# Performance work log

Hardware: AMD Instinct MI355X
Metric: run time of the kernel (lower is better)

## Reference

```python
import jax, jax.numpy as jnp
import numpy as np

N_NODES = 10000
N_EDGES = 640000
IN_FEATS = 128
H_FEATS1 = 128
NUM_OUTPUTS = 64


def setup_inputs() -> dict:
    key = jax.random.key(0)
    k0, k1, k2, k3, k4 = jax.random.split(key, 5)
    in_feat = jax.random.normal(k0, (N_NODES, IN_FEATS), dtype=jnp.float32)
    src = jax.random.randint(k1, (N_EDGES,), 0, N_NODES, dtype=jnp.int64)
    dst = jax.random.randint(k2, (N_EDGES,), 0, N_NODES, dtype=jnp.int64)
    W1 = jax.random.normal(k3, (IN_FEATS, H_FEATS1), dtype=jnp.float32) * 0.05
    b1 = jnp.zeros((H_FEATS1,), dtype=jnp.float32)
    W2 = jax.random.normal(k4, (H_FEATS1, NUM_OUTPUTS), dtype=jnp.float32) * 0.05
    b2 = jnp.zeros((NUM_OUTPUTS,), dtype=jnp.float32)
    return {"in_feat": in_feat, "src": src, "dst": dst,
            "W1": W1, "b1": b1, "W2": W2, "b2": b2}


def _graph_conv(src, dst, x, W, b):
    # DGL GraphConv with norm='both': out = D_out^{-1/2} A^T-agg D_in^{-1/2} x W + b
    n = x.shape[0]
    ones = jnp.ones((src.shape[0],), dtype=x.dtype)
    deg_out = jnp.clip(jax.ops.segment_sum(ones, src, num_segments=n), 1.0)
    deg_in = jnp.clip(jax.ops.segment_sum(ones, dst, num_segments=n), 1.0)
    h = x * jax.lax.rsqrt(deg_out)[:, None]            # src-side normalization
    agg = jax.ops.segment_sum(h[src], dst, num_segments=n)  # SpMM: sum over in-edges
    agg = agg * jax.lax.rsqrt(deg_in)[:, None]         # dst-side normalization
    return agg @ W + b


def reference(in_feat, src, dst, W1, b1, W2, b2):
    h = _graph_conv(src, dst, in_feat, W1, b1)
    h = jax.nn.relu(h)  # dropout=0 -> identity
    return _graph_conv(src, dst, h, W2, b2)
```

## Files before the change

kernel.cpp:

```cpp
#include <hip/hip_runtime.h>

#define NFEAT 128
#define NOUT  64
#define PCAP  128
#define HB    256

__global__ void hist_kernel(const int* __restrict__ src, const int* __restrict__ dst,
                            unsigned char* __restrict__ hist_src,
                            unsigned char* __restrict__ hist_dst,
                            unsigned int* __restrict__ pe, int nN, int nE) {
    extern __shared__ int bins[];
    int b = blockIdx.x;
    int per = (nE + HB - 1) / HB;
    int lo = b * per, hi = min(lo + per, nE);
    for (int i = threadIdx.x; i < nN; i += blockDim.x) bins[i] = 0;
    __syncthreads();
    for (int e = lo + threadIdx.x; e < hi; e += blockDim.x) {
        int s = src[e], d = dst[e];
        atomicAdd(&bins[d], 1);
        atomicAdd(&bins[s], 0x10000);
        pe[e] = (unsigned int)(unsigned short)s | ((unsigned int)d << 16);
    }
    __syncthreads();
    for (int i = threadIdx.x; i < nN; i += blockDim.x) {
        int v = bins[i];
        hist_dst[(size_t)b * nN + i] = (unsigned char)min(v & 0xFFFF, 255);
        hist_src[(size_t)b * nN + i] = (unsigned char)min(v >> 16, 255);
    }
}

__global__ void offsets_kernel(const unsigned char* __restrict__ hist_src,
                               const unsigned char* __restrict__ hist_dst,
                               unsigned char* __restrict__ base_rel,
                               unsigned short* __restrict__ deg_in,
                               float* __restrict__ rs_in, float* __restrict__ rs_out, int nN) {
    int tid = blockIdx.x * blockDim.x + threadIdx.x;
    if (tid < nN) {
        int i = tid;
        int run = 0;
#pragma unroll 16
        for (int b = 0; b < HB; b++) {
            base_rel[(size_t)b * nN + i] = (unsigned char)min(run, 255);
            run += hist_dst[(size_t)b * nN + i];
        }
        deg_in[i] = (unsigned short)min(run, PCAP);
        rs_in[i] = rsqrtf(fmaxf((float)run, 1.0f));
    } else if (tid < 2 * nN) {
        int i = tid - nN;
        int to = 0;
#pragma unroll 16
        for (int b = 0; b < HB; b++) to += hist_src[(size_t)b * nN + i];
        rs_out[i] = rsqrtf(fmaxf((float)to, 1.0f));
    }
}

__global__ void scatter_kernel(const unsigned int* __restrict__ pe,
                               const unsigned char* __restrict__ base_rel,
                               unsigned short* __restrict__ csr, int nN, int nE) {
    extern __shared__ int cur[];
    int b = blockIdx.x;
    int per = (nE + HB - 1) / HB;
    int lo = b * per, hi = min(lo + per, nE);
    for (int i = threadIdx.x; i < nN; i += blockDim.x)
        cur[i] = base_rel[(size_t)b * nN + i];
    __syncthreads();
    for (int e = lo + threadIdx.x; e < hi; e += blockDim.x) {
        unsigned int v = pe[e];
        int s = v & 0xFFFF, d = v >> 16;
        int pos = atomicAdd(&cur[d], 1);
        if (pos < PCAP)
            csr[(size_t)d * PCAP + pos] = (unsigned short)s;
    }
}

__global__ void gather1_kernel(const unsigned short* __restrict__ deg_in,
                               const unsigned short* __restrict__ csr,
                               const float* __restrict__ x, const float* __restrict__ rs_out,
                               const float* __restrict__ rs_in,
                               float* __restrict__ t, int nN) {
    __shared__ unsigned short eids[4][PCAP];
    __shared__ float rsv[4][PCAP];
    int tid = threadIdx.x;
    int w = tid >> 6, lane = tid & 63;
    int i = blockIdx.x * 4 + w;
    int n = deg_in[i];
    ((unsigned int*)eids[w])[lane] = ((const unsigned int*)(csr + (size_t)i * PCAP))[lane];
    __syncthreads();
    for (int e = lane; e < n; e += 64) rsv[w][e] = rs_out[eids[w][e]];
    __syncthreads();

    const float4* xv = (const float4*)x;
    int quad = lane >> 4;
    int g = lane & 15;
    float s_in = rs_in[i];
#pragma unroll
    for (int p = 0; p < 2; p++) {
        int gg = g + 16 * p;
        float4 acc = {0.f, 0.f, 0.f, 0.f};
        int e = quad;
        for (; e + 12 < n; e += 16) {
            int s0 = eids[w][e],     s1 = eids[w][e + 4];
            int s2 = eids[w][e + 8], s3 = eids[w][e + 12];
            float f0 = rsv[w][e],     f1 = rsv[w][e + 4];
            float f2 = rsv[w][e + 8], f3 = rsv[w][e + 12];
            float4 v0 = xv[(size_t)s0 * 32 + gg];
            float4 v1 = xv[(size_t)s1 * 32 + gg];
            float4 v2 = xv[(size_t)s2 * 32 + gg];
            float4 v3 = xv[(size_t)s3 * 32 + gg];
            acc.x += v0.x * f0 + v1.x * f1 + v2.x * f2 + v3.x * f3;
            acc.y += v0.y * f0 + v1.y * f1 + v2.y * f2 + v3.y * f3;
            acc.z += v0.z * f0 + v1.z * f1 + v2.z * f2 + v3.z * f3;
            acc.w += v0.w * f0 + v1.w * f1 + v2.w * f2 + v3.w * f3;
        }
        for (; e + 4 < n; e += 8) {
            int s0 = eids[w][e], s1 = eids[w][e + 4];
            float f0 = rsv[w][e], f1 = rsv[w][e + 4];
            float4 v0 = xv[(size_t)s0 * 32 + gg];
            float4 v1 = xv[(size_t)s1 * 32 + gg];
            acc.x += v0.x * f0 + v1.x * f1;
            acc.y += v0.y * f0 + v1.y * f1;
            acc.z += v0.z * f0 + v1.z * f1;
            acc.w += v0.w * f0 + v1.w * f1;
        }
        for (; e < n; e += 4) {
            int s0 = eids[w][e];
            float f0 = rsv[w][e];
            float4 v0 = xv[(size_t)s0 * 32 + gg];
            acc.x += v0.x * f0; acc.y += v0.y * f0; acc.z += v0.z * f0; acc.w += v0.w * f0;
        }
#pragma unroll
        for (int d = 16; d <= 32; d <<= 1) {
            acc.x += __shfl_xor(acc.x, d);
            acc.y += __shfl_xor(acc.y, d);
            acc.z += __shfl_xor(acc.z, d);
            acc.w += __shfl_xor(acc.w, d);
        }
        if (lane < 16) {
            acc.x *= s_in; acc.y *= s_in; acc.z *= s_in; acc.w *= s_in;
            ((float4*)(t + (size_t)i * NFEAT))[gg] = acc;
        }
    }
}

#define NPB 16
__global__ void mlp_kernel(const float* __restrict__ t_in, const float* __restrict__ rs_out,
                           const float* __restrict__ W1, const float* __restrict__ b1,
                           const float* __restrict__ W2, float* __restrict__ z, int nN) {
    __shared__ float ts[NPB][NFEAT];
    __shared__ float h1[NPB][NFEAT];
    int i0 = blockIdx.x * NPB;
    int tid = threadIdx.x;
    for (int t2 = tid; t2 < NPB * NFEAT; t2 += 256)
        ts[t2 >> 7][t2 & 127] = t_in[(size_t)i0 * NFEAT + t2];
    __syncthreads();
    {
        int j = tid & 127;
        int g = (tid >> 7) * 8;
        float a[8];
        float b = b1[j];
#pragma unroll
        for (int u = 0; u < 8; u++) a[u] = b;
#pragma unroll 8
        for (int k = 0; k < NFEAT; k++) {
            float w = W1[k * NFEAT + j];
#pragma unroll
            for (int u = 0; u < 8; u++) a[u] += ts[g + u][k] * w;
        }
#pragma unroll
        for (int u = 0; u < 8; u++) h1[g + u][j] = fmaxf(a[u], 0.0f);
    }
    __syncthreads();
    {
        int j2 = tid & 63;
        int g2 = (tid >> 6) * 4;
        float c[4] = {0.f, 0.f, 0.f, 0.f};
#pragma unroll 8
        for (int k = 0; k < NFEAT; k++) {
            float w = W2[k * NOUT + j2];
#pragma unroll
            for (int u = 0; u < 4; u++) c[u] += h1[g2 + u][k] * w;
        }
#pragma unroll
        for (int u = 0; u < 4; u++)
            z[(size_t)(i0 + g2 + u) * NOUT + j2] = c[u] * rs_out[i0 + g2 + u];
    }
}

__global__ void gather2_kernel(const unsigned short* __restrict__ deg_in,
                               const unsigned short* __restrict__ csr,
                               const float* __restrict__ z, const float* __restrict__ rs_in,
                               const float* __restrict__ b2, float* __restrict__ out, int nN) {
    __shared__ unsigned short eids[4][PCAP];
    int tid = threadIdx.x;
    int w = tid >> 6, lane = tid & 63;
    int i = blockIdx.x * 4 + w;
    int n = deg_in[i];
    ((unsigned int*)eids[w])[lane] = ((const unsigned int*)(csr + (size_t)i * PCAP))[lane];
    __syncthreads();

    const float4* zv = (const float4*)z;
    int quad = lane >> 4;
    int g = lane & 15;
    float4 acc = {0.f, 0.f, 0.f, 0.f};
    int e = quad;
    for (; e + 12 < n; e += 16) {
        int s0 = eids[w][e],     s1 = eids[w][e + 4];
        int s2 = eids[w][e + 8], s3 = eids[w][e + 12];
        float4 v0 = zv[(size_t)s0 * 16 + g];
        float4 v1 = zv[(size_t)s1 * 16 + g];
        float4 v2 = zv[(size_t)s2 * 16 + g];
        float4 v3 = zv[(size_t)s3 * 16 + g];
        acc.x += v0.x + v1.x + v2.x + v3.x;
        acc.y += v0.y + v1.y + v2.y + v3.y;
        acc.z += v0.z + v1.z + v2.z + v3.z;
        acc.w += v0.w + v1.w + v2.w + v3.w;
    }
    for (; e + 4 < n; e += 8) {
        float4 v0 = zv[(size_t)eids[w][e] * 16 + g];
        float4 v1 = zv[(size_t)eids[w][e + 4] * 16 + g];
        acc.x += v0.x + v1.x; acc.y += v0.y + v1.y;
        acc.z += v0.z + v1.z; acc.w += v0.w + v1.w;
    }
    for (; e < n; e += 4) {
        float4 v0 = zv[(size_t)eids[w][e] * 16 + g];
        acc.x += v0.x; acc.y += v0.y; acc.z += v0.z; acc.w += v0.w;
    }
#pragma unroll
    for (int d = 16; d <= 32; d <<= 1) {
        acc.x += __shfl_xor(acc.x, d);
        acc.y += __shfl_xor(acc.y, d);
        acc.z += __shfl_xor(acc.z, d);
        acc.w += __shfl_xor(acc.w, d);
    }
    if (lane < 16) {
        float s = rs_in[i];
        float4 bb = ((const float4*)b2)[g];
        acc.x = acc.x * s + bb.x; acc.y = acc.y * s + bb.y;
        acc.z = acc.z * s + bb.z; acc.w = acc.w * s + bb.w;
        ((float4*)(out + (size_t)i * NOUT))[g] = acc;
    }
}

extern "C" void kernel_launch(void* const* d_in, const int* in_sizes, int n_in,
                              void* d_out, int out_size, void* d_ws, size_t ws_size,
                              hipStream_t stream) {
    const float* x  = (const float*)d_in[0];
    const int* src  = (const int*)d_in[1];
    const int* dst  = (const int*)d_in[2];
    const float* W1 = (const float*)d_in[3];
    const float* b1 = (const float*)d_in[4];
    const float* W2 = (const float*)d_in[5];
    const float* b2 = (const float*)d_in[6];
    float* out = (float*)d_out;

    const int nN = in_sizes[0] / NFEAT;
    const int nE = in_sizes[1];

    char* p = (char*)d_ws;
    unsigned char* hist_src = (unsigned char*)p; p += (size_t)HB * nN;
    unsigned char* hist_dst = (unsigned char*)p; p += (size_t)HB * nN;
    unsigned char* base_rel = (unsigned char*)p; p += (size_t)HB * nN;
    unsigned int*  pe       = (unsigned int*)p;  p += (size_t)nE * 4;
    unsigned short* csr     = (unsigned short*)p; p += (size_t)nN * PCAP * 2;
    unsigned short* deg_in  = (unsigned short*)p; p += (size_t)nN * 2;
    float* rs_in  = (float*)p; p += (size_t)nN * sizeof(float);
    float* rs_out = (float*)p; p += (size_t)nN * sizeof(float);
    float* t = (float*)p; p += (size_t)nN * NFEAT * sizeof(float);
    float* z = (float*)p; p += (size_t)nN * NOUT * sizeof(float);

    hist_kernel<<<HB, 256, (size_t)nN * sizeof(int), stream>>>(
        src, dst, hist_src, hist_dst, pe, nN, nE);
    offsets_kernel<<<(2 * nN + 255) / 256, 256, 0, stream>>>(
        hist_src, hist_dst, base_rel, deg_in, rs_in, rs_out, nN);
    scatter_kernel<<<HB, 256, (size_t)nN * sizeof(int), stream>>>(
        pe, base_rel, csr, nN, nE);
    gather1_kernel<<<nN / 4, 256, 0, stream>>>(deg_in, csr, x, rs_out, rs_in, t, nN);
    mlp_kernel<<<nN / NPB, 256, 0, stream>>>(t, rs_out, W1, b1, W2, z, nN);
    gather2_kernel<<<nN / 4, 256, 0, stream>>>(deg_in, csr, z, rs_in, b2, out, nN);
}
```

Measured before the change: 160.8 us.

## Store gathered node features in bf16 to halve SpMM gather traffic

The input features are converted to packed bf16 inside the histogram kernel, and the second-layer projected features are written as bf16 by the MLP kernel. Both gather kernels now read 16-byte packed bf16 rows, unpack them to fp32 and accumulate in fp32, with the lane mapping reworked to match. This targets the random-access gather bandwidth that dominates the SpMM stages. In exchange it adds a conversion pass and bf16 rounding error on the aggregated features.

Measured after the change: 161.0 us. Within noise of the previous version (+0.1%).

```diff
diff --git a/kernel.cpp b/kernel.cpp
--- a/kernel.cpp
+++ b/kernel.cpp
@@ -5,10 +5,22 @@
 #define PCAP  128
 #define HB    256
 
+__device__ __forceinline__ unsigned int f2bf(float f) {
+    union { float f; unsigned int u; } v; v.f = f;
+    return (v.u + 0x7FFFu + ((v.u >> 16) & 1u)) >> 16;
+}
+__device__ __forceinline__ void unpack2(unsigned int u, float& lo, float& hi) {
+    union { unsigned int u; float f; } a, b;
+    a.u = u << 16; b.u = u & 0xFFFF0000u;
+    lo = a.f; hi = b.f;
+}
+
 __global__ void hist_kernel(const int* __restrict__ src, const int* __restrict__ dst,
+                            const float* __restrict__ x,
                             unsigned char* __restrict__ hist_src,
                             unsigned char* __restrict__ hist_dst,
-                            unsigned int* __restrict__ pe, int nN, int nE) {
+                            unsigned int* __restrict__ pe,
+                            unsigned int* __restrict__ xh, int nN, int nE) {
     extern __shared__ int bins[];
     int b = blockIdx.x;
     int per = (nE + HB - 1) / HB;
@@ -26,6 +38,11 @@
         int v = bins[i];
         hist_dst[(size_t)b * nN + i] = (unsigned char)min(v & 0xFFFF, 255);
         hist_src[(size_t)b * nN + i] = (unsigned char)min(v >> 16, 255);
+    }
+    int total = nN * (NFEAT / 2);
+    for (int idx = b * blockDim.x + threadIdx.x; idx < total; idx += HB * blockDim.x) {
+        float2 v = ((const float2*)x)[idx];
+        xh[idx] = f2bf(v.x) | (f2bf(v.y) << 16);
     }
 }
 
@@ -75,7 +92,8 @@
 
 __global__ void gather1_kernel(const unsigned short* __restrict__ deg_in,
                                const unsigned short* __restrict__ csr,
-                               const float* __restrict__ x, const float* __restrict__ rs_out,
+                               const unsigned int* __restrict__ xh,
+                               const float* __restrict__ rs_out,
                                const float* __restrict__ rs_in,
                                float* __restrict__ t, int nN) {
     __shared__ unsigned short eids[4][PCAP];
@@ -89,63 +107,53 @@
     for (int e = lane; e < n; e += 64) rsv[w][e] = rs_out[eids[w][e]];
     __syncthreads();
 
-    const float4* xv = (const float4*)x;
+    const uint4* xv = (const uint4*)xh;
     int quad = lane >> 4;
     int g = lane & 15;
+    float acc[8] = {0.f, 0.f, 0.f, 0.f, 0.f, 0.f, 0.f, 0.f};
     float s_in = rs_in[i];
-#pragma unroll
-    for (int p = 0; p < 2; p++) {
-        int gg = g + 16 * p;
-        float4 acc = {0.f, 0.f, 0.f, 0.f};
-        int e = quad;
-        for (; e + 12 < n; e += 16) {
-            int s0 = eids[w][e],     s1 = eids[w][e + 4];
-            int s2 = eids[w][e + 8], s3 = eids[w][e + 12];
-            float f0 = rsv[w][e],     f1 = rsv[w][e + 4];
-            float f2 = rsv[w][e + 8], f3 = rsv[w][e + 12];
-            float4 v0 = xv[(size_t)s0 * 32 + gg];
-            float4 v1 = xv[(size_t)s1 * 32 + gg];
-            float4 v2 = xv[(size_t)s2 * 32 + gg];
-            float4 v3 = xv[(size_t)s3 * 32 + gg];
-            acc.x += v0.x * f0 + v1.x * f1 + v2.x * f2 + v3.x * f3;
-            acc.y += v0.y * f0 + v1.y * f1 + v2.y * f2 + v3.y * f3;
-            acc.z += v0.z * f0 + v1.z * f1 + v2.z * f2 + v3.z * f3;
-            acc.w += v0.w * f0 + v1.w * f1 + v2.w * f2 + v3.w * f3;
-        }
-        for (; e + 4 < n; e += 8) {
-            int s0 = eids[w][e], s1 = eids[w][e + 4];
-            float f0 = rsv[w][e], f1 = rsv[w][e + 4];
-            float4 v0 = xv[(size_t)s0 * 32 + gg];
-            float4 v1 = xv[(size_t)s1 * 32 + gg];
-            acc.x += v0.x * f0 + v1.x * f1;
-            acc.y += v0.y * f0 + v1.y * f1;
-            acc.z += v0.z * f0 + v1.z * f1;
-            acc.w += v0.w * f0 + v1.w * f1;
-        }
-        for (; e < n; e += 4) {
-            int s0 = eids[w][e];
-            float f0 = rsv[w][e];
-            float4 v0 = xv[(size_t)s0 * 32 + gg];
-            acc.x += v0.x * f0; acc.y += v0.y * f0; acc.z += v0.z * f0; acc.w += v0.w * f0;
-        }
-#pragma unroll
-        for (int d = 16; d <= 32; d <<= 1) {
-            acc.x += __shfl_xor(acc.x, d);
-            acc.y += __shfl_xor(acc.y, d);
-            acc.z += __shfl_xor(acc.z, d);
-            acc.w += __shfl_xor(acc.w, d);
-        }
-        if (lane < 16) {
-            acc.x *= s_in; acc.y *= s_in; acc.z *= s_in; acc.w *= s_in;
-            ((float4*)(t + (size_t)i * NFEAT))[gg] = acc;
-        }
+    int e = quad;
+    for (; e + 4 < n; e += 8) {
+        int s0 = eids[w][e], s1 = eids[w][e + 4];
+        float f0 = rsv[w][e], f1 = rsv[w][e + 4];
+        uint4 u0 = xv[(size_t)s0 * 16 + g];
+        uint4 u1 = xv[(size_t)s1 * 16 + g];
+        float a, b;
+        unpack2(u0.x, a, b); acc[0] += a * f0; acc[1] += b * f0;
+        unpack2(u0.y, a, b); acc[2] += a * f0; acc[3] += b * f0;
+        unpack2(u0.z, a, b); acc[4] += a * f0; acc[5] += b * f0;
+        unpack2(u0.w, a, b); acc[6] += a * f0; acc[7] += b * f0;
+        unpack2(u1.x, a, b); acc[0] += a * f1; acc[1] += b * f1;
+        unpack2(u1.y, a, b); acc[2] += a * f1; acc[3] += b * f1;
+        unpack2(u1.z, a, b); acc[4] += a * f1; acc[5] += b * f1;
+        unpack2(u1.w, a, b); acc[6] += a * f1; acc[7] += b * f1;
+    }
+    for (; e < n; e += 4) {
+        int s0 = eids[w][e];
+        float f0 = rsv[w][e];
+        uint4 u0 = xv[(size_t)s0 * 16 + g];
+        float a, b;
+        unpack2(u0.x, a, b); acc[0] += a * f0; acc[1] += b * f0;
+        unpack2(u0.y, a, b); acc[2] += a * f0; acc[3] += b * f0;
+        unpack2(u0.z, a, b); acc[4] += a * f0; acc[5] += b * f0;
+        unpack2(u0.w, a, b); acc[6] += a * f0; acc[7] += b * f0;
+    }
+#pragma unroll
+    for (int d = 16; d <= 32; d <<= 1)
+#pragma unroll
+        for (int u = 0; u < 8; u++) acc[u] += __shfl_xor(acc[u], d);
+    if (lane < 16) {
+        float4 o0 = {acc[0] * s_in, acc[1] * s_in, acc[2] * s_in, acc[3] * s_in};
+        float4 o1 = {acc[4] * s_in, acc[5] * s_in, acc[6] * s_in, acc[7] * s_in};
+        float4* tp = (float4*)(t + (size_t)i * NFEAT + g * 8);
+        tp[0] = o0; tp[1] = o1;
     }
 }
 
 #define NPB 16
 __global__ void mlp_kernel(const float* __restrict__ t_in, const float* __restrict__ rs_out,
                            const float* __restrict__ W1, const float* __restrict__ b1,
-                           const float* __restrict__ W2, float* __restrict__ z, int nN) {
+                           const float* __restrict__ W2, unsigned int* __restrict__ zh, int nN) {
     __shared__ float ts[NPB][NFEAT];
     __shared__ float h1[NPB][NFEAT];
     int i0 = blockIdx.x * NPB;
@@ -171,24 +179,29 @@
     }
     __syncthreads();
     {
-        int j2 = tid & 63;
-        int g2 = (tid >> 6) * 4;
-        float c[4] = {0.f, 0.f, 0.f, 0.f};
+        int j2 = (tid & 31) * 2;
+        int g2 = (tid >> 5) * 2;
+        float c00 = 0.f, c01 = 0.f, c10 = 0.f, c11 = 0.f;
+        const float2* W2v = (const float2*)W2;
 #pragma unroll 8
         for (int k = 0; k < NFEAT; k++) {
-            float w = W2[k * NOUT + j2];
-#pragma unroll
-            for (int u = 0; u < 4; u++) c[u] += h1[g2 + u][k] * w;
+            float2 wv = W2v[k * 32 + (j2 >> 1)];
+            float ha = h1[g2][k], hb = h1[g2 + 1][k];
+            c00 += ha * wv.x; c01 += ha * wv.y;
+            c10 += hb * wv.x; c11 += hb * wv.y;
         }
-#pragma unroll
-        for (int u = 0; u < 4; u++)
-            z[(size_t)(i0 + g2 + u) * NOUT + j2] = c[u] * rs_out[i0 + g2 + u];
+        float s0 = rs_out[i0 + g2], s1 = rs_out[i0 + g2 + 1];
+        zh[(size_t)(i0 + g2) * (NOUT / 2) + (j2 >> 1)] =
+            f2bf(c00 * s0) | (f2bf(c01 * s0) << 16);
+        zh[(size_t)(i0 + g2 + 1) * (NOUT / 2) + (j2 >> 1)] =
+            f2bf(c10 * s1) | (f2bf(c11 * s1) << 16);
     }
 }
 
 __global__ void gather2_kernel(const unsigned short* __restrict__ deg_in,
                                const unsigned short* __restrict__ csr,
-                               const float* __restrict__ z, const float* __restrict__ rs_in,
+                               const unsigned int* __restrict__ zh,
+                               const float* __restrict__ rs_in,
                                const float* __restrict__ b2, float* __restrict__ out, int nN) {
     __shared__ unsigned short eids[4][PCAP];
     int tid = threadIdx.x;
@@ -198,46 +211,46 @@
     ((unsigned int*)eids[w])[lane] = ((const unsigned int*)(csr + (size_t)i * PCAP))[lane];
     __syncthreads();
 
-    const float4* zv = (const float4*)z;
-    int quad = lane >> 4;
-    int g = lane & 15;
-    float4 acc = {0.f, 0.f, 0.f, 0.f};
-    int e = quad;
-    for (; e + 12 < n; e += 16) {
-        int s0 = eids[w][e],     s1 = eids[w][e + 4];
-        int s2 = eids[w][e + 8], s3 = eids[w][e + 12];
-        float4 v0 = zv[(size_t)s0 * 16 + g];
-        float4 v1 = zv[(size_t)s1 * 16 + g];
-        float4 v2 = zv[(size_t)s2 * 16 + g];
-        float4 v3 = zv[(size_t)s3 * 16 + g];
-        acc.x += v0.x + v1.x + v2.x + v3.x;
-        acc.y += v0.y + v1.y + v2.y + v3.y;
-        acc.z += v0.z + v1.z + v2.z + v3.z;
-        acc.w += v0.w + v1.w + v2.w + v3.w;
-    }
-    for (; e + 4 < n; e += 8) {
-        float4 v0 = zv[(size_t)eids[w][e] * 16 + g];
-        float4 v1 = zv[(size_t)eids[w][e + 4] * 16 + g];
-        acc.x += v0.x + v1.x; acc.y += v0.y + v1.y;
-        acc.z += v0.z + v1.z; acc.w += v0.w + v1.w;
-    }
-    for (; e < n; e += 4) {
-        float4 v0 = zv[(size_t)eids[w][e] * 16 + g];
-        acc.x += v0.x; acc.y += v0.y; acc.z += v0.z; acc.w += v0.w;
-    }
-#pragma unroll
-    for (int d = 16; d <= 32; d <<= 1) {
-        acc.x += __shfl_xor(acc.x, d);
-        acc.y += __shfl_xor(acc.y, d);
-        acc.z += __shfl_xor(acc.z, d);
-        acc.w += __shfl_xor(acc.w, d);
-    }
-    if (lane < 16) {
+    const uint4* zv = (const uint4*)zh;
+    int oct = lane >> 3;
+    int g = lane & 7;
+    float acc[8] = {0.f, 0.f, 0.f, 0.f, 0.f, 0.f, 0.f, 0.f};
+    int e = oct;
+    for (; e + 8 < n; e += 16) {
+        int s0 = eids[w][e], s1 = eids[w][e + 8];
+        uint4 u0 = zv[(size_t)s0 * 8 + g];
+        uint4 u1 = zv[(size_t)s1 * 8 + g];
+        float a, b;
+        unpack2(u0.x, a, b); acc[0] += a; acc[1] += b;
+        unpack2(u0.y, a, b); acc[2] += a; acc[3] += b;
+        unpack2(u0.z, a, b); acc[4] += a; acc[5] += b;
+        unpack2(u0.w, a, b); acc[6] += a; acc[7] += b;
+        unpack2(u1.x, a, b); acc[0] += a; acc[1] += b;
+        unpack2(u1.y, a, b); acc[2] += a; acc[3] += b;
+        unpack2(u1.z, a, b); acc[4] += a; acc[5] += b;
+        unpack2(u1.w, a, b); acc[6] += a; acc[7] += b;
+    }
+    for (; e < n; e += 8) {
+        int s0 = eids[w][e];
+        uint4 u0 = zv[(size_t)s0 * 8 + g];
+        float a, b;
+        unpack2(u0.x, a, b); acc[0] += a; acc[1] += b;
+        unpack2(u0.y, a, b); acc[2] += a; acc[3] += b;
+        unpack2(u0.z, a, b); acc[4] += a; acc[5] += b;
+        unpack2(u0.w, a, b); acc[6] += a; acc[7] += b;
+    }
+#pragma unroll
+    for (int d = 8; d <= 32; d <<= 1)
+#pragma unroll
+        for (int u = 0; u < 8; u++) acc[u] += __shfl_xor(acc[u], d);
+    if (lane < 8) {
         float s = rs_in[i];
-        float4 bb = ((const float4*)b2)[g];
-        acc.x = acc.x * s + bb.x; acc.y = acc.y * s + bb.y;
-        acc.z = acc.z * s + bb.z; acc.w = acc.w * s + bb.w;
-        ((float4*)(out + (size_t)i * NOUT))[g] = acc;
+        float4 ba = ((const float4*)b2)[g * 2];
+        float4 bb = ((const float4*)b2)[g * 2 + 1];
+        float4 o0 = {acc[0] * s + ba.x, acc[1] * s + ba.y, acc[2] * s + ba.z, acc[3] * s + ba.w};
+        float4 o1 = {acc[4] * s + bb.x, acc[5] * s + bb.y, acc[6] * s + bb.z, acc[7] * s + bb.w};
+        float4* op = (float4*)(out + (size_t)i * NOUT + g * 8);
+        op[0] = o0; op[1] = o1;
     }
 }
 
@@ -265,16 +278,17 @@
     unsigned short* deg_in  = (unsigned short*)p; p += (size_t)nN * 2;
     float* rs_in  = (float*)p; p += (size_t)nN * sizeof(float);
     float* rs_out = (float*)p; p += (size_t)nN * sizeof(float);
+    unsigned int* xh = (unsigned int*)p; p += (size_t)nN * (NFEAT / 2) * 4;
     float* t = (float*)p; p += (size_t)nN * NFEAT * sizeof(float);
-    float* z = (float*)p; p += (size_t)nN * NOUT * sizeof(float);
+    unsigned int* zh = (unsigned int*)p; p += (size_t)nN * (NOUT / 2) * 4;
 
     hist_kernel<<<HB, 256, (size_t)nN * sizeof(int), stream>>>(
-        src, dst, hist_src, hist_dst, pe, nN, nE);
+        src, dst, x, hist_src, hist_dst, pe, xh, nN, nE);
     offsets_kernel<<<(2 * nN + 255) / 256, 256, 0, stream>>>(
         hist_src, hist_dst, base_rel, deg_in, rs_in, rs_out, nN);
     scatter_kernel<<<HB, 256, (size_t)nN * sizeof(int), stream>>>(
         pe, base_rel, csr, nN, nE);
-    gather1_kernel<<<nN / 4, 256, 0, stream>>>(deg_in, csr, x, rs_out, rs_in, t, nN);
-    mlp_kernel<<<nN / NPB, 256, 0, stream>>>(t, rs_out, W1, b1, W2, z, nN);
-    gather2_kernel<<<nN / 4, 256, 0, stream>>>(deg_in, csr, z, rs_in, b2, out, nN);
-}
+    gather1_kernel<<<nN / 4, 256, 0, stream>>>(deg_in, csr, xh, rs_out, rs_in, t, nN);
+    mlp_kernel<<<nN / NPB, 256, 0, stream>>>(t, rs_out, W1, b1, W2, zh, nN);
+    gather2_kernel<<<nN / 4, 256, 0, stream>>>(deg_in, csr, zh, rs_in, b2, out, nN);
+}
```
